# Kernel optimization log

Hardware: AMD Instinct MI355X
Metric: run time of the kernel (lower is better)

The kernel has to match this reference:

```python
import jax, jax.numpy as jnp
import numpy as np
from jax import lax

VOCAB, MAX_LEN, EMB, H = 50000, 128, 300, 50
BATCH = 1024
BN_SCALE = 1.0 / np.sqrt(1.0 + 0.001)  # batch_normalization with mean=0, var=1, eps=1e-3


def setup_inputs() -> dict:
    key = jax.random.key(0)
    ks = jax.random.split(key, 10)
    return {
        "x1": jax.random.randint(ks[0], (BATCH, MAX_LEN), 0, VOCAB, dtype=jnp.int32),
        "x2": jax.random.randint(ks[1], (BATCH, MAX_LEN), 0, VOCAB, dtype=jnp.int32),
        "embedding_matrix": jax.random.normal(ks[2], (VOCAB, EMB), jnp.float32),
        "W_fw": jax.random.normal(ks[3], (EMB + H, 4 * H), jnp.float32) * 0.05,
        "b_fw": jnp.zeros((4 * H,), jnp.float32),
        "W_bw": jax.random.normal(ks[4], (EMB + H, 4 * H), jnp.float32) * 0.05,
        "b_bw": jnp.zeros((4 * H,), jnp.float32),
        "W1": jax.random.normal(ks[5], (2 * H, 25), jnp.float32) * 0.1,
        "b1": jax.random.normal(ks[6], (25,), jnp.float32) * 0.1,
        "W2": jax.random.normal(ks[7], (25, 3), jnp.float32) * 0.1,
        "b2": jax.random.normal(ks[8], (3,), jnp.float32) * 0.1,
    }


def _lstm_scan(xs, W, b):
    # xs: [T, B, E]; BasicLSTMCell: gates = [x, h] @ W + b, split i, j, f, o; forget_bias=1.0
    T, B, _ = xs.shape
    def step(carry, x):
        c, h = carry
        g = jnp.concatenate([x, h], axis=-1) @ W + b
        i, j, f, o = jnp.split(g, 4, axis=-1)
        c2 = c * jax.nn.sigmoid(f + 1.0) + jax.nn.sigmoid(i) * jnp.tanh(j)
        h2 = jnp.tanh(c2) * jax.nn.sigmoid(o)
        return (c2, h2), h2
    init = (jnp.zeros((B, H), xs.dtype), jnp.zeros((B, H), xs.dtype))
    _, hs = lax.scan(step, init, xs)
    return hs  # [T, B, H]


def reference(x1, x2, embedding_matrix, W_fw, b_fw, W_bw, b_bw, W1, b1, W2, b2):
    tokens = jnp.concatenate([x1, x2], axis=1)            # [B, 2*max_len]
    emb = embedding_matrix[tokens]                         # [B, T, E]
    xs = jnp.transpose(emb, (1, 0, 2))                     # [T, B, E]
    h_fw = _lstm_scan(xs, W_fw, b_fw)                      # [T, B, H]
    h_bw = _lstm_scan(xs[::-1], W_bw, b_bw)                # [T, B, H] (time reversed)
    # static_bidirectional_rnn reverses bw outputs, so outputs[-1] pairs
    # fw at step T-1 with bw's first step (which consumed x_{T-1}).
    feat = jnp.concatenate([h_fw[-1], h_bw[0]], axis=-1)   # [B, 2H]
    bn = feat * BN_SCALE
    h1 = jax.nn.relu(bn @ W1 + b1)                         # dropout omitted (eval mode)
    out = h1 @ W2 + b2
    return out * BN_SCALE
```

## Files before the change

kernel.cpp:

```cpp
#include <hip/hip_runtime.h>
#include <hip/hip_bf16.h>


#define VOCAB 50000
#define EMB   300
#define HID   50
#define GATES 200
#define BATCH 1024
#define TT    256
#define BN_SCALE 0.9995003746877732f

__device__ __forceinline__ float sigm(float x) {
    return 1.0f / (1.0f + __expf(-x));
}
__device__ __forceinline__ float tanh_f(float x) {
    return 1.0f - 2.0f / (__expf(2.0f * x) + 1.0f);
}

__global__ __launch_bounds__(256) void vocab_proj(const float* __restrict__ E,
                                                  const float* __restrict__ Wx,
                                                  float* __restrict__ P) {
    __shared__ __align__(16) float sE[32 * EMB];
    const int v0 = blockIdx.x * 32;
    const int t  = threadIdx.x;

    const int base = v0 * EMB;
    const int vmax = VOCAB * EMB;
    for (int idx = t; idx < 32 * EMB; idx += 256) {
        int g = base + idx;
        sE[idx] = (g < vmax) ? E[g] : 0.0f;
    }
    __syncthreads();
    if (t >= GATES) return;

    float acc[32];
#pragma unroll
    for (int r = 0; r < 32; ++r) acc[r] = 0.0f;

    for (int e = 0; e < EMB; e += 4) {
        const float w0 = Wx[(e + 0) * GATES + t];
        const float w1 = Wx[(e + 1) * GATES + t];
        const float w2 = Wx[(e + 2) * GATES + t];
        const float w3 = Wx[(e + 3) * GATES + t];
#pragma unroll
        for (int r = 0; r < 32; ++r) {
            const float4 ev = *reinterpret_cast<const float4*>(&sE[r * EMB + e]);
            acc[r] = fmaf(ev.w, w3, fmaf(ev.z, w2, fmaf(ev.y, w1, fmaf(ev.x, w0, acc[r]))));
        }
    }
#pragma unroll
    for (int r = 0; r < 32; ++r) {
        const int v = v0 + r;
        if (v < VOCAB) P[v * GATES + t] = acc[r];
    }
}

__global__ __launch_bounds__(256) void lstm_fw(const int* __restrict__ x1,
                                               const int* __restrict__ x2,
                                               const float* __restrict__ P,
                                               const float* __restrict__ Wfw,
                                               const float* __restrict__ bfw,
                                               float* __restrict__ feat) {
    const int b = blockIdx.x;
    const int j = threadIdx.x;

    __shared__ float sh[HID];
    __shared__ float sg[GATES];

    float whh[HID];
    float bj = 0.0f;
    if (j < GATES) {
        bj = bfw[j];
#pragma unroll
        for (int k = 0; k < HID; ++k)
            whh[k] = Wfw[(EMB + k) * GATES + j];
    }
    float c = 0.0f;
    if (j < HID) sh[j] = 0.0f;
    __syncthreads();

    int tok0 = x1[b * 128];
    float pf = (j < GATES) ? P[tok0 * GATES + j] : 0.0f;

    for (int t = 0; t < TT; ++t) {
        float pfn = 0.0f;
        if (t < TT - 1) {
            const int tn   = t + 1;
            const int tokn = (tn < 128) ? x1[b * 128 + tn] : x2[b * 128 + tn - 128];
            if (j < GATES) pfn = P[tokn * GATES + j];
        }

        if (j < GATES) {
            float g0 = pf + bj, g1 = 0.0f;
#pragma unroll
            for (int k = 0; k < HID; k += 2) {
                g0 = fmaf(whh[k],     sh[k],     g0);
                g1 = fmaf(whh[k + 1], sh[k + 1], g1);
            }
            sg[j] = g0 + g1;
        }
        __syncthreads();

        if (j < HID) {
            const float gi = sg[j];
            const float gj = sg[j + HID];
            const float gf = sg[j + 2 * HID];
            const float go = sg[j + 3 * HID];
            c = c * sigm(gf + 1.0f) + sigm(gi) * tanh_f(gj);
            sh[j] = tanh_f(c) * sigm(go);
        }
        __syncthreads();
        pf = pfn;
    }

    if (j < HID) feat[b * (2 * HID) + j] = sh[j];
}

__global__ __launch_bounds__(256) void bw_mlp(const int* __restrict__ x2,
                                              const float* __restrict__ E,
                                              const float* __restrict__ Wbw,
                                              const float* __restrict__ bbw,
                                              const float* __restrict__ W1,
                                              const float* __restrict__ b1,
                                              const float* __restrict__ W2,
                                              const float* __restrict__ b2,
                                              const float* __restrict__ featfw,
                                              float* __restrict__ out) {
    const int b = blockIdx.x;
    const int t = threadIdx.x;

    __shared__ __align__(16) float sx[EMB + 4];
    __shared__ float sf[2 * HID];
    __shared__ float sg[GATES];
    __shared__ float sh1[25];

    const int tok = x2[b * 128 + 127];
    for (int e = t; e < EMB; e += 256) sx[e] = E[tok * EMB + e];
    if (t < HID) sf[t] = featfw[b * (2 * HID) + t];
    __syncthreads();

    if (t < GATES) {
        float g0 = bbw[t], g1 = 0.0f, g2 = 0.0f, g3 = 0.0f;
        for (int e = 0; e < EMB; e += 4) {
            g0 = fmaf(sx[e + 0], Wbw[(e + 0) * GATES + t], g0);
            g1 = fmaf(sx[e + 1], Wbw[(e + 1) * GATES + t], g1);
            g2 = fmaf(sx[e + 2], Wbw[(e + 2) * GATES + t], g2);
            g3 = fmaf(sx[e + 3], Wbw[(e + 3) * GATES + t], g3);
        }
        sg[t] = (g0 + g1) + (g2 + g3);
    }
    __syncthreads();

    if (t < HID) {
        const float c2 = sigm(sg[t]) * tanh_f(sg[t + HID]);
        sf[HID + t] = tanh_f(c2) * sigm(sg[t + 3 * HID]);
    }
    __syncthreads();

    if (t < 25) {
        float a = 0.0f;
#pragma unroll 4
        for (int k = 0; k < 2 * HID; ++k)
            a = fmaf(sf[k], W1[k * 25 + t], a);
        a = fmaf(a, BN_SCALE, b1[t]);
        sh1[t] = fmaxf(a, 0.0f);
    }
    __syncthreads();

    if (t < 3) {
        float a = b2[t];
#pragma unroll
        for (int k = 0; k < 25; ++k)
            a = fmaf(sh1[k], W2[k * 3 + t], a);
        out[b * 3 + t] = a * BN_SCALE;
    }
}

extern "C" void kernel_launch(void* const* d_in, const int* in_sizes, int n_in,
                              void* d_out, int out_size, void* d_ws, size_t ws_size,
                              hipStream_t stream) {
    const int*   x1  = (const int*)d_in[0];
    const int*   x2  = (const int*)d_in[1];
    const float* E   = (const float*)d_in[2];
    const float* Wfw = (const float*)d_in[3];
    const float* bfw = (const float*)d_in[4];
    const float* Wbw = (const float*)d_in[5];
    const float* bbw = (const float*)d_in[6];
    const float* W1  = (const float*)d_in[7];
    const float* b1  = (const float*)d_in[8];
    const float* W2  = (const float*)d_in[9];
    const float* b2  = (const float*)d_in[10];
    float* out = (float*)d_out;

    float* P    = (float*)d_ws;
    float* feat = P + (size_t)VOCAB * GATES;

    vocab_proj<<<(VOCAB + 31) / 32, 256, 0, stream>>>(E, Wfw, P);
    lstm_fw<<<BATCH, 256, 0, stream>>>(x1, x2, P, Wfw, bfw, feat);
    bw_mlp<<<BATCH, 256, 0, stream>>>(x2, E, Wbw, bbw, W1, b1, W2, b2, feat, out);
}
```

Measured before the change: 454.8 us.

## Run forward LSTM in one wavefront per sequence using shuffles, drop shared staging

The forward LSTM kernel now uses a single 64-lane wavefront per batch row, and each lane computes all four gates for one hidden unit. The hidden state is broadcast with lane shuffles instead of shared memory, which removes both block barriers per timestep. Token ids are staged in shared memory, and precomputed input projections are double-buffered two steps ahead. The vocab projection kernel no longer stages embeddings in shared memory; it reads them directly from global memory through the cache, which may cost more memory traffic in that kernel.

```diff
diff --git a/kernel.cpp b/kernel.cpp
--- a/kernel.cpp
+++ b/kernel.cpp
@@ -20,100 +20,107 @@
 __global__ __launch_bounds__(256) void vocab_proj(const float* __restrict__ E,
                                                   const float* __restrict__ Wx,
                                                   float* __restrict__ P) {
-    __shared__ __align__(16) float sE[32 * EMB];
     const int v0 = blockIdx.x * 32;
     const int t  = threadIdx.x;
 
-    const int base = v0 * EMB;
-    const int vmax = VOCAB * EMB;
-    for (int idx = t; idx < 32 * EMB; idx += 256) {
-        int g = base + idx;
-        sE[idx] = (g < vmax) ? E[g] : 0.0f;
-    }
-    __syncthreads();
-    if (t >= GATES) return;
-
     float acc[32];
 #pragma unroll
     for (int r = 0; r < 32; ++r) acc[r] = 0.0f;
 
-    for (int e = 0; e < EMB; e += 4) {
-        const float w0 = Wx[(e + 0) * GATES + t];
-        const float w1 = Wx[(e + 1) * GATES + t];
-        const float w2 = Wx[(e + 2) * GATES + t];
-        const float w3 = Wx[(e + 3) * GATES + t];
+    if (t < GATES) {
+        for (int e = 0; e < EMB; e += 4) {
+            const float w0 = Wx[(e + 0) * GATES + t];
+            const float w1 = Wx[(e + 1) * GATES + t];
+            const float w2 = Wx[(e + 2) * GATES + t];
+            const float w3 = Wx[(e + 3) * GATES + t];
+#pragma unroll
+            for (int r = 0; r < 32; ++r) {
+                const int vr = (v0 + r < VOCAB) ? (v0 + r) : (VOCAB - 1);
+                const float* Er = E + (size_t)vr * EMB + e;
+                acc[r] = fmaf(Er[3], w3, fmaf(Er[2], w2,
+                         fmaf(Er[1], w1, fmaf(Er[0], w0, acc[r]))));
+            }
+        }
 #pragma unroll
         for (int r = 0; r < 32; ++r) {
-            const float4 ev = *reinterpret_cast<const float4*>(&sE[r * EMB + e]);
-            acc[r] = fmaf(ev.w, w3, fmaf(ev.z, w2, fmaf(ev.y, w1, fmaf(ev.x, w0, acc[r]))));
-        }
-    }
-#pragma unroll
-    for (int r = 0; r < 32; ++r) {
-        const int v = v0 + r;
-        if (v < VOCAB) P[v * GATES + t] = acc[r];
-    }
-}
-
-__global__ __launch_bounds__(256) void lstm_fw(const int* __restrict__ x1,
-                                               const int* __restrict__ x2,
-                                               const float* __restrict__ P,
-                                               const float* __restrict__ Wfw,
-                                               const float* __restrict__ bfw,
-                                               float* __restrict__ feat) {
+            const int v = v0 + r;
+            if (v < VOCAB) P[(size_t)v * GATES + t] = acc[r];
+        }
+    }
+}
+
+#define LSTM_STEP(PI, PJ, PF, PO, TNEXT)                                      \
+    {                                                                         \
+        float ai = PI + bi0, aj = PJ + bj0, af = PF + bf0, ao = PO + bo0;     \
+        {                  \
+            const int tk = stok[TNEXT];                                       \
+            const float* pr = P + (size_t)tk * GATES + u;                     \
+            PI = pr[0]; PJ = pr[50]; PF = pr[100]; PO = pr[150];              \
+        }                                                                     \
+        _Pragma("unroll")                                                     \
+        for (int k = 0; k < HID; ++k) {                                       \
+            const float hk = __shfl(h, k);                                    \
+            ai = fmaf(wi[k], hk, ai);                                         \
+            aj = fmaf(wj[k], hk, aj);                                         \
+            af = fmaf(wf[k], hk, af);                                         \
+            ao = fmaf(wo[k], hk, ao);                                         \
+        }                                                                     \
+        c = c * sigm(af + 1.0f) + sigm(ai) * tanh_f(aj);                      \
+        h = tanh_f(c) * sigm(ao);                                             \
+    }
+
+__global__ __launch_bounds__(64, 1) void lstm_fw(const int* __restrict__ x1,
+                                                 const int* __restrict__ x2,
+                                                 const float* __restrict__ P,
+                                                 const float* __restrict__ Wfw,
+                                                 const float* __restrict__ bfw,
+                                                 float* __restrict__ feat) {
     const int b = blockIdx.x;
-    const int j = threadIdx.x;
-
-    __shared__ float sh[HID];
-    __shared__ float sg[GATES];
-
-    float whh[HID];
-    float bj = 0.0f;
-    if (j < GATES) {
-        bj = bfw[j];
-#pragma unroll
-        for (int k = 0; k < HID; ++k)
-            whh[k] = Wfw[(EMB + k) * GATES + j];
-    }
-    float c = 0.0f;
-    if (j < HID) sh[j] = 0.0f;
-    __syncthreads();
-
-    int tok0 = x1[b * 128];
-    float pf = (j < GATES) ? P[tok0 * GATES + j] : 0.0f;
-
-    for (int t = 0; t < TT; ++t) {
-        float pfn = 0.0f;
-        if (t < TT - 1) {
-            const int tn   = t + 1;
-            const int tokn = (tn < 128) ? x1[b * 128 + tn] : x2[b * 128 + tn - 128];
-            if (j < GATES) pfn = P[tokn * GATES + j];
-        }
-
-        if (j < GATES) {
-            float g0 = pf + bj, g1 = 0.0f;
-#pragma unroll
-            for (int k = 0; k < HID; k += 2) {
-                g0 = fmaf(whh[k],     sh[k],     g0);
-                g1 = fmaf(whh[k + 1], sh[k + 1], g1);
-            }
-            sg[j] = g0 + g1;
-        }
-        __syncthreads();
-
-        if (j < HID) {
-            const float gi = sg[j];
-            const float gj = sg[j + HID];
-            const float gf = sg[j + 2 * HID];
-            const float go = sg[j + 3 * HID];
-            c = c * sigm(gf + 1.0f) + sigm(gi) * tanh_f(gj);
-            sh[j] = tanh_f(c) * sigm(go);
-        }
-        __syncthreads();
-        pf = pfn;
-    }
-
-    if (j < HID) feat[b * (2 * HID) + j] = sh[j];
+    const int u = threadIdx.x;
+
+    __shared__ int stok[TT];
+    for (int i = u; i < 128; i += 64) {
+        stok[i]       = x1[b * 128 + i];
+        stok[128 + i] = x2[b * 128 + i];
+    }
+    __syncthreads();
+
+    if (u < HID) {
+        float wi[HID], wj[HID], wf[HID], wo[HID];
+        const float bi0 = bfw[u];
+        const float bj0 = bfw[u + 50];
+        const float bf0 = bfw[u + 100];
+        const float bo0 = bfw[u + 150];
+#pragma unroll
+        for (int k = 0; k < HID; ++k) {
+            const float* row = Wfw + (size_t)(EMB + k) * GATES;
+            wi[k] = row[u];
+            wj[k] = row[u + 50];
+            wf[k] = row[u + 100];
+            wo[k] = row[u + 150];
+        }
+
+        float c = 0.0f, h = 0.0f;
+
+        float pAi, pAj, pAf, pAo, pBi, pBj, pBf, pBo;
+        {
+            const float* pr = P + (size_t)stok[0] * GATES + u;
+            pAi = pr[0]; pAj = pr[50]; pAf = pr[100]; pAo = pr[150];
+        }
+        {
+            const float* pr = P + (size_t)stok[1] * GATES + u;
+            pBi = pr[0]; pBj = pr[50]; pBf = pr[100]; pBo = pr[150];
+        }
+
+        for (int t = 0; t < TT; t += 2) {
+            const int n2 = (t + 2 < TT) ? t + 2 : TT - 1;
+            const int n3 = (t + 3 < TT) ? t + 3 : TT - 1;
+            LSTM_STEP(pAi, pAj, pAf, pAo, n2);
+            LSTM_STEP(pBi, pBj, pBf, pBo, n3);
+        }
+
+        feat[b * (2 * HID) + u] = h;
+    }
 }
 
 __global__ __launch_bounds__(256) void bw_mlp(const int* __restrict__ x2,
@@ -135,7 +142,7 @@
     __shared__ float sh1[25];
 
     const int tok = x2[b * 128 + 127];
-    for (int e = t; e < EMB; e += 256) sx[e] = E[tok * EMB + e];
+    for (int e = t; e < EMB; e += 256) sx[e] = E[(size_t)tok * EMB + e];
     if (t < HID) sf[t] = featfw[b * (2 * HID) + t];
     __syncthreads();
 
@@ -192,10 +199,10 @@
     const float* b2  = (const float*)d_in[10];
     float* out = (float*)d_out;
 
-    float* P    = (float*)d_ws;
-    float* feat = P + (size_t)VOCAB * GATES;
-
-    vocab_proj<<<(VOCAB + 31) / 32, 256, 0, stream>>>(E, Wfw, P);
-    lstm_fw<<<BATCH, 256, 0, stream>>>(x1, x2, P, Wfw, bfw, feat);
+    float* Pm   = (float*)d_ws;
+    float* feat = Pm + (size_t)VOCAB * GATES;
+
+    vocab_proj<<<(VOCAB + 31) / 32, 256, 0, stream>>>(E, Wfw, Pm);
+    lstm_fw<<<BATCH, 64, 0, stream>>>(x1, x2, Pm, Wfw, bfw, feat);
     bw_mlp<<<BATCH, 256, 0, stream>>>(x2, E, Wbw, bbw, W1, b1, W2, b2, feat, out);
 }
```

After: 1.049 ms. 131% more time.
